# Performance work log

Hardware: AMD Instinct MI355X
Metric: run time of the kernel (lower is better)

## Reference

```python
import jax, jax.numpy as jnp
import numpy as np

DECAY = 0.99
EPSILON = 1e-05
BETA = 0.25  # vq_commitment_beta


def setup_inputs() -> dict:
    key = jax.random.key(0)
    k1, k2, k3, k4 = jax.random.split(key, 4)
    N, dim, K = 32768, 512, 8192
    init_range = 1.0 / np.sqrt(dim)
    emb_w = jax.random.uniform(k3, (K, 2 * dim), dtype=jnp.float32,
                               minval=-init_range, maxval=init_range)
    return {
        "z_real": jax.random.normal(k1, (N, dim), dtype=jnp.float32),
        "z_imag": jax.random.normal(k2, (N, dim), dtype=jnp.float32),
        "emb_w": emb_w,
        "ema_cluster_size": jnp.zeros((K,), dtype=jnp.float32),
        "ema_w": emb_w.copy(),
    }


def reference(z_real, z_imag, emb_w, ema_cluster_size, ema_w):
    N, dim = z_real.shape
    K = emb_w.shape[0]
    z_flat = jnp.concatenate([z_real, z_imag], axis=-1)  # [N, 2*dim]

    # squared euclidean distances [N, K]
    x_sq = jnp.sum(z_flat * z_flat, axis=1, keepdims=True)
    y_sq = jnp.sum(emb_w * emb_w, axis=1)
    d = jnp.maximum(x_sq + y_sq - 2.0 * (z_flat @ emb_w.T), 0.0)
    indices = jnp.argmin(d, axis=-1)  # [N]
    z_q = emb_w[indices]              # [N, 2*dim]

    # EMA codebook update (training-mode buffer math, no grads)
    n_total = jnp.zeros((K,), z_flat.dtype).at[indices].add(1.0)
    new_cluster_size = ema_cluster_size * DECAY + (1.0 - DECAY) * n_total
    cs = new_cluster_size + EPSILON
    cs = cs + (cs < 1.0).astype(cs.dtype)
    dw = jnp.zeros((K, 2 * dim), z_flat.dtype).at[indices].add(z_flat)  # encodings.T @ z_flat
    new_ema_w = ema_w * DECAY + (1.0 - DECAY) * dw
    new_w = jnp.clip(new_ema_w / cs[:, None], -5.0, 5.0)

    loss_sample = BETA * jnp.mean((z_q - z_flat) ** 2, axis=-1)  # [N]

    # straight-through (forward value == z_q)
    z_q_st = z_flat + jax.lax.stop_gradient(z_q - z_flat)

    probs = n_total / N
    norm_entropy = -jnp.sum(probs * jnp.log(probs + 1e-10)) / np.log(float(K))

    z_q_r = z_q_st[..., :dim]
    z_q_i = z_q_st[..., dim:]
    return (z_q_r, z_q_i, loss_sample, indices, norm_entropy,
            new_w, new_cluster_size, new_ema_w)
```

## Files before the change

kernel.cpp:

```cpp
#include <hip/hip_runtime.h>
#include <hip/hip_bf16.h>

#define NROWS 32768
#define DIM   512
#define D2    1024
#define KCODE 8192
#define DECAYF 0.99f
#define OMD    0.01f
#define CANDCAP 16
#define ZMAX 6.0f
#define IRANGE 0.04419417382415922f
#define MARGIN_P (9200 << 7)

typedef __attribute__((ext_vector_type(4))) int   v4i;
typedef __attribute__((ext_vector_type(16))) int  i32x16;

#define WS_EMB8T   0u
#define WS_YSQ     8388608u
#define WS_NINT    8421376u
#define WS_ENT     8454144u
#define WS_FIDX    10682384u
#define WS_OFF     10813456u
#define WS_CUR     10846224u
#define WS_ROWLIST 10878992u

#define OUT_ZQR  0
#define OUT_ZQI  16777216
#define OUT_LOSS 33554432
#define OUT_IDX  33587200
#define OUT_ENT  33619968
#define OUT_NEWW 33619969
#define OUT_NCS  42008577
#define OUT_NEMA 42016769
#define PAIRS_OFF (OUT_NEWW + 1)

__device__ __forceinline__ float wredf(float v) {
    #pragma unroll
    for (int o = 32; o > 0; o >>= 1) v += __shfl_down(v, o, 64);
    return v;
}

__device__ __forceinline__ double wredd(double v) {
    #pragma unroll
    for (int o = 32; o > 0; o >>= 1) v += __shfl_down(v, o, 64);
    return __shfl(v, 0, 64);
}

__device__ __forceinline__ double ulp32_of(double v) {
    return scalbn(1.0, ilogb(v) - 23);
}

__device__ __forceinline__ void gload_lds16(const void* g, void* l) {
    __builtin_amdgcn_global_load_lds(
        (const __attribute__((address_space(1))) unsigned int*)(g),
        (__attribute__((address_space(3))) unsigned int*)(l), 16, 0, 0);
}

__device__ __forceinline__ int q4(float4 v, float s) {
    int a = (int)rintf(fminf(fmaxf(v.x * s, -127.f), 127.f));
    int b = (int)rintf(fminf(fmaxf(v.y * s, -127.f), 127.f));
    int c = (int)rintf(fminf(fmaxf(v.z * s, -127.f), 127.f));
    int d = (int)rintf(fminf(fmaxf(v.w * s, -127.f), 127.f));
    return (a & 255) | ((b & 255) << 8) | ((c & 255) << 16) | ((d & 255) << 24);
}

__global__ __launch_bounds__(256) void prep_emb(const float* __restrict__ emb,
                                                char* __restrict__ emb8t,
                                                int* __restrict__ ysq) {
    int wave = threadIdx.x >> 6, lane = threadIdx.x & 63;
    int k = blockIdx.x * 4 + wave;
    const float4* src = (const float4*)(emb + (size_t)k * D2);
    const float es = 127.0f / IRANGE;
    const float sfac_inv = 1.0f / (2.0f * (ZMAX / 127.0f) * (IRANGE / 127.0f));
    float s = 0.f;
    float4 v0 = src[lane * 4 + 0];
    float4 v1 = src[lane * 4 + 1];
    float4 v2 = src[lane * 4 + 2];
    float4 v3 = src[lane * 4 + 3];
    s += v0.x*v0.x + v0.y*v0.y + v0.z*v0.z + v0.w*v0.w;
    s += v1.x*v1.x + v1.y*v1.y + v1.z*v1.z + v1.w*v1.w;
    s += v2.x*v2.x + v2.y*v2.y + v2.z*v2.z + v2.w*v2.w;
    s += v3.x*v3.x + v3.y*v3.y + v3.z*v3.z + v3.w*v3.w;
    v4i pk; pk[0] = q4(v0, es); pk[1] = q4(v1, es); pk[2] = q4(v2, es); pk[3] = q4(v3, es);
    v4i* dst = (v4i*)(emb8t + (size_t)(k >> 5) * 32768 + (size_t)lane * 512 + (k & 31) * 16);
    *dst = pk;
    s = wredf(s);
    if (lane == 0) ysq[k] = (int)rintf(s * sfac_inv);
}

__global__ __launch_bounds__(512, 2) void argmin_gemm(
    const float* __restrict__ zr, const float* __restrict__ zi,
    const char* __restrict__ emb8t, const int* __restrict__ ysq,
    long long* __restrict__ pairs)
{
    __shared__ char bufs[2][65536];
    const int tid  = threadIdx.x;
    const int wave = tid >> 6, lane = tid & 63;
    const int colc = lane & 31;
    const int hh   = lane >> 5;
    const int rowblk = blockIdx.x >> 1;
    const int slice  = blockIdx.x & 1;

    const int arow = rowblk * 256 + wave * 32 + colc;
    const float zs = 127.0f / ZMAX;
    const float* zrp = zr + (size_t)arow * 512 + hh * 16;
    const float* zip = zi + (size_t)arow * 512 + hh * 16;
    v4i afrag[32];
    #pragma unroll
    for (int ft = 0; ft < 16; ++ft) {
        const float4* p = (const float4*)(zrp + ft * 32);
        v4i a; a[0] = q4(p[0], zs); a[1] = q4(p[1], zs); a[2] = q4(p[2], zs); a[3] = q4(p[3], zs);
        afrag[ft] = a;
    }
    #pragma unroll
    for (int ft = 0; ft < 16; ++ft) {
        const float4* p = (const float4*)(zip + ft * 32);
        v4i a; a[0] = q4(p[0], zs); a[1] = q4(p[1], zs); a[2] = q4(p[2], zs); a[3] = q4(p[3], zs);
        afrag[16 + ft] = a;
    }

    int tv0[16], tv1[16];
    #pragma unroll
    for (int g = 0; g < 16; ++g) { tv0[g] = 0x7FFFFFFF; tv1[g] = 0x7FFFFFFF; }

    const char* gslice = emb8t + (size_t)slice * 128 * 32768;
    const int* yslice = ysq + slice * 4096;

#define STAGE(dstbuf, c_) do {                                                   \
        const char* gb = gslice + (size_t)(c_) * 65536 + wave * 8192             \
                       + (size_t)lane * 16;                                      \
        char* lb = (dstbuf) + wave * 8192;                                       \
        _Pragma("unroll")                                                        \
        for (int q = 0; q < 8; ++q)                                              \
            gload_lds16(gb + q * 1024, lb + q * 1024);                           \
    } while (0)

    const int boff = colc * 16 + hh * 512;

    STAGE(bufs[0], 0);
    __syncthreads();

    for (int c = 0; c < 64; ++c) {
        const int cur = c & 1;
        if (c + 1 < 64) STAGE(bufs[cur ^ 1], c + 1);
        int ysA = yslice[c * 64 + colc];
        int ysB = yslice[c * 64 + 32 + colc];

        const char* bb = &bufs[cur][0] + boff;
        i32x16 accA, accB;
        #pragma unroll
        for (int g = 0; g < 16; ++g) { accA[g] = 0; accB[g] = 0; }
        __builtin_amdgcn_s_setprio(1);
        #pragma unroll
        for (int m = 0; m < 32; ++m) {
            v4i bA = *(const v4i*)(bb + m * 1024);
            v4i bB = *(const v4i*)(bb + m * 1024 + 32768);
            accA = __builtin_amdgcn_mfma_i32_32x32x32_i8(afrag[m], bA, accA, 0, 0, 0);
            accB = __builtin_amdgcn_mfma_i32_32x32x32_i8(afrag[m], bB, accB, 0, 0, 0);
        }
        __builtin_amdgcn_s_setprio(0);

        const int idA = c * 2, idB = c * 2 + 1;
        #pragma unroll
        for (int g = 0; g < 16; ++g) {
            int pkA = ((ysA - accA[g]) << 7) | idA;
            tv1[g] = min(tv1[g], max(pkA, tv0[g]));
            tv0[g] = min(tv0[g], pkA);
            int pkB = ((ysB - accB[g]) << 7) | idB;
            tv1[g] = min(tv1[g], max(pkB, tv0[g]));
            tv0[g] = min(tv0[g], pkB);
        }
        __syncthreads();
    }
#undef STAGE

    #pragma unroll
    for (int g = 0; g < 16; ++g) {
        int rloc = (g & 3) + 8 * (g >> 2) + 4 * hh;
        int rowg = rowblk * 256 + wave * 32 + rloc;
        size_t base = (size_t)rowg * 128 + slice * 64 + colc * 2;
        int t0 = tv0[g], t1 = tv1[g];
        int code0 = slice * 4096 + (t0 & 127) * 32 + colc;
        int code1 = slice * 4096 + (t1 & 127) * 32 + colc;
        pairs[base + 0] = ((long long)(unsigned)code0 << 32) | (unsigned)t0;
        pairs[base + 1] = ((long long)(unsigned)code1 << 32) | (unsigned)t1;
    }
}

__global__ __launch_bounds__(256) void cleanup(
    const float* __restrict__ zr, const float* __restrict__ zi,
    const float* __restrict__ emb, const long long* __restrict__ pairs,
    int* __restrict__ fidx, int* __restrict__ nint, float* __restrict__ out)
{
    __shared__ int candlds[4][CANDCAP];
    int wave = threadIdx.x >> 6, lane = threadIdx.x & 63;
    int r = blockIdx.x * 4 + wave;

    const long long* pr = pairs + (size_t)r * 128;
    long long p0 = pr[lane];
    long long p1 = pr[64 + lane];
    int v0v = (int)(unsigned)p0;
    int i0  = (int)(p0 >> 32);
    int v1v = (int)(unsigned)p1;
    int i1  = (int)(p1 >> 32);
    int m = min(v0v, v1v);
    #pragma unroll
    for (int o = 32; o > 0; o >>= 1) m = min(m, __shfl_xor(m, o, 64));
    int lim = m + MARGIN_P;
    unsigned long long m0 = __ballot(v0v < lim);
    unsigned long long m1 = __ballot(v1v < lim);
    int t0 = __popcll(m0);
    int cnt = t0 + __popcll(m1);
    if (cnt > CANDCAP) cnt = CANDCAP;
    unsigned long long below = (lane == 63) ? 0xFFFFFFFFFFFFFFFFull >> 1
                                            : ((1ull << lane) - 1);
    if (v0v < lim) {
        int pos = __popcll(m0 & below);
        if (pos < CANDCAP) candlds[wave][pos] = i0;
    }
    if (v1v < lim) {
        int pos = t0 + __popcll(m1 & below);
        if (pos < CANDCAP) candlds[wave][pos] = i1;
    }
    int best = candlds[wave][0];

    float zreg[16];
    #pragma unroll
    for (int p = 0; p < 4; ++p) {
        int d4 = p * 64 + lane;
        const float4* zp = (d4 < 128) ? (const float4*)(zr + (size_t)r * 512)
                                      : ((const float4*)(zi + (size_t)r * 512) - 128);
        float4 zv = zp[d4];
        zreg[p * 4 + 0] = zv.x; zreg[p * 4 + 1] = zv.y;
        zreg[p * 4 + 2] = zv.z; zreg[p * 4 + 3] = zv.w;
    }

    if (cnt > 1) {
        double xs = 0.0;
        #pragma unroll
        for (int j = 0; j < 16; ++j) xs += (double)zreg[j] * (double)zreg[j];
        xs = wredd(xs);
        double uS = ulp32_of(xs);

        double bD = 1e300; int bi = 1 << 30;
        for (int i = 0; i < cnt; ++i) {
            int cdx = candlds[wave][i];
            const float4* ep = (const float4*)(emb + (size_t)cdx * 1024);
            double ys = 0.0, tt = 0.0;
            #pragma unroll
            for (int p = 0; p < 4; ++p) {
                float4 ev = ep[p * 64 + lane];
                float q0 = ev.x * ev.x, q1 = ev.y * ev.y, q2 = ev.z * ev.z, q3 = ev.w * ev.w;
                ys += (double)q0 + (double)q1 + (double)q2 + (double)q3;
                tt += (double)zreg[p * 4 + 0] * (double)ev.x
                    + (double)zreg[p * 4 + 1] * (double)ev.y
                    + (double)zreg[p * 4 + 2] * (double)ev.z
                    + (double)zreg[p * 4 + 3] * (double)ev.w;
            }
            ys = wredd(ys);
            tt = wredd(tt);
            float y32 = (float)ys;
            float t32 = (float)tt;
            double dex = xs + ys - 2.0 * tt;
            double ud = ulp32_of(dex);
            double D = rint((double)y32 / uS) * uS - rint(2.0 * (double)t32 / ud) * ud;
            if (D < bD || (D == bD && cdx < bi)) { bD = D; bi = cdx; }
        }
        best = bi;
    }

    const float4* ep = (const float4*)(emb + (size_t)best * 1024);
    float acc = 0.f;
    #pragma unroll
    for (int p = 0; p < 4; ++p) {
        int d4 = p * 64 + lane;
        float4 ev = ep[d4];
        float dx = ev.x - zreg[p * 4 + 0]; acc += dx * dx;
        float dy = ev.y - zreg[p * 4 + 1]; acc += dy * dy;
        float dz = ev.z - zreg[p * 4 + 2]; acc += dz * dz;
        float dw = ev.w - zreg[p * 4 + 3]; acc += dw * dw;
        float4* op = (d4 < 128) ? (float4*)(out + OUT_ZQR + (size_t)r * 512)
                                : ((float4*)(out + OUT_ZQI + (size_t)r * 512) - 128);
        op[d4] = ev;
    }
    acc = wredf(acc);
    if (lane == 0) {
        fidx[r] = best;
        out[OUT_IDX + r] = (float)best;
        out[OUT_LOSS + r] = 0.25f * acc * (1.f / 1024.f);
        atomicAdd(nint + best, 1);
    }
}

__global__ __launch_bounds__(256) void scan_codes(const int* __restrict__ nint,
                                                  int* __restrict__ off,
                                                  int* __restrict__ cur) {
    __shared__ int part[256];
    int tid = threadIdx.x;
    int base = tid * 32;
    int loc[32];
    int s = 0;
    #pragma unroll
    for (int j = 0; j < 32; ++j) { loc[j] = s; s += nint[base + j]; }
    part[tid] = s;
    __syncthreads();
    for (int o = 1; o < 256; o <<= 1) {
        int t = (tid >= o) ? part[tid - o] : 0;
        __syncthreads();
        part[tid] += t;
        __syncthreads();
    }
    int excl = part[tid] - s;
    #pragma unroll
    for (int j = 0; j < 32; ++j) {
        off[base + j] = excl + loc[j];
        cur[base + j] = 0;
    }
}

__global__ __launch_bounds__(256) void fill_rows(const int* __restrict__ fidx,
                                                 const int* __restrict__ off,
                                                 int* __restrict__ cur,
                                                 int* __restrict__ rowlist) {
    int r = blockIdx.x * 256 + threadIdx.x;
    int idx = fidx[r];
    int pos = atomicAdd(cur + idx, 1);
    rowlist[off[idx] + pos] = r;
}

__global__ __launch_bounds__(256) void ema_update(
    const float* __restrict__ zr, const float* __restrict__ zi,
    const float* __restrict__ emaw, const float* __restrict__ emacs,
    const int* __restrict__ nint, const int* __restrict__ off,
    const int* __restrict__ rowlist, float* __restrict__ out,
    float* __restrict__ entacc)
{
    int k = blockIdx.x;
    int tid = threadIdx.x;
    int cnt = nint[k];
    int o0 = off[k];
    float ax = 0.f, ay = 0.f, az = 0.f, aw = 0.f;
    for (int i = 0; i < cnt; ++i) {
        int r = rowlist[o0 + i];
        float4 zv = (tid < 128) ? ((const float4*)(zr + (size_t)r * 512))[tid]
                                : ((const float4*)(zi + (size_t)r * 512))[tid - 128];
        ax += zv.x; ay += zv.y; az += zv.z; aw += zv.w;
    }
    float4 ew = ((const float4*)(emaw + (size_t)k * 1024))[tid];
    float4 nem;
    nem.x = DECAYF * ew.x + OMD * ax;
    nem.y = DECAYF * ew.y + OMD * ay;
    nem.z = DECAYF * ew.z + OMD * az;
    nem.w = DECAYF * ew.w + OMD * aw;
    ((float4*)(out + OUT_NEMA + (size_t)k * 1024))[tid] = nem;
    float ncs = DECAYF * emacs[k] + OMD * (float)cnt;
    float cs = ncs + 1e-5f;
    if (cs < 1.f) cs += 1.f;
    float inv = 1.f / cs;
    float4 w;
    w.x = fminf(fmaxf(nem.x * inv, -5.f), 5.f);
    w.y = fminf(fmaxf(nem.y * inv, -5.f), 5.f);
    w.z = fminf(fmaxf(nem.z * inv, -5.f), 5.f);
    w.w = fminf(fmaxf(nem.w * inv, -5.f), 5.f);
    ((float4*)(out + OUT_NEWW + (size_t)k * 1024))[tid] = w;
    if (tid == 0) {
        out[OUT_NCS + k] = ncs;
        float p = (float)cnt / 32768.f;
        atomicAdd(entacc, -p * logf(p + 1e-10f));
    }
}

__global__ void ent_fin(const float* __restrict__ entacc, float* __restrict__ out) {
    if (threadIdx.x == 0) out[OUT_ENT] = entacc[0] / logf(8192.f);
}

extern "C" void kernel_launch(void* const* d_in, const int* in_sizes, int n_in,
                              void* d_out, int out_size, void* d_ws, size_t ws_size,
                              hipStream_t stream)
{
    const float* zr    = (const float*)d_in[0];
    const float* zi    = (const float*)d_in[1];
    const float* emb   = (const float*)d_in[2];
    const float* emacs = (const float*)d_in[3];
    const float* emaw  = (const float*)d_in[4];
    float* out = (float*)d_out;
    char* ws = (char*)d_ws;

    char*  emb8t   = (char*)(ws + WS_EMB8T);
    int*   ysq     = (int*)(ws + WS_YSQ);
    int*   nint    = (int*)(ws + WS_NINT);
    float* entacc  = (float*)(ws + WS_ENT);
    int*   fidx    = (int*)(ws + WS_FIDX);
    int*   off     = (int*)(ws + WS_OFF);
    int*   cur     = (int*)(ws + WS_CUR);
    int*   rowlist = (int*)(ws + WS_ROWLIST);
    long long* pairs = (long long*)(out + PAIRS_OFF);

    hipMemsetAsync(ws + WS_NINT, 0, 32768 + 16, stream);

    prep_emb   <<<2048, 256, 0, stream>>>(emb, emb8t, ysq);
    argmin_gemm<<<256,  512, 0, stream>>>(zr, zi, emb8t, ysq, pairs);
    cleanup    <<<8192, 256, 0, stream>>>(zr, zi, emb, pairs, fidx, nint, out);
    scan_codes <<<1,    256, 0, stream>>>(nint, off, cur);
    fill_rows  <<<128,  256, 0, stream>>>(fidx, off, cur, rowlist);
    ema_update <<<8192, 256, 0, stream>>>(zr, zi, emaw, emacs, nint, off, rowlist, out, entacc);
    ent_fin    <<<1,    64,  0, stream>>>(entacc, out);
}
```

Baseline: 518.1 us.

## Deepen argmin GEMM pipeline to four smaller LDS stages with split-K accumulators

The codebook staging in the int8 argmin GEMM moves from a double buffer of 64KB tiles to a 4-deep ring of 32KB tiles, each holding 32 codes. Each iteration now waits on vmcnt with a single barrier instead of a full __syncthreads pair, and keeps three loads in flight. The K dimension is split over two independent accumulators (even and odd k-steps) that are summed afterwards, so consecutive MFMAs do not depend on each other. The loop runs 128 iterations with half the work each, which adds barrier overhead per MFMA. The prefetch past the last tile wraps around and reloads tile 0, which is harmless but adds redundant loads.

```diff
diff --git a/kernel.cpp b/kernel.cpp
--- a/kernel.cpp
+++ b/kernel.cpp
@@ -93,7 +93,7 @@
     const char* __restrict__ emb8t, const int* __restrict__ ysq,
     long long* __restrict__ pairs)
 {
-    __shared__ char bufs[2][65536];
+    __shared__ char bufs[4][32768];
     const int tid  = threadIdx.x;
     const int wave = tid >> 6, lane = tid & 63;
     const int colc = lane & 31;
@@ -126,51 +126,49 @@
     const char* gslice = emb8t + (size_t)slice * 128 * 32768;
     const int* yslice = ysq + slice * 4096;
 
-#define STAGE(dstbuf, c_) do {                                                   \
-        const char* gb = gslice + (size_t)(c_) * 65536 + wave * 8192             \
+#define STAGE(bidx_, t_) do {                                                    \
+        const char* gb = gslice + (size_t)(t_) * 32768 + wave * 4096             \
                        + (size_t)lane * 16;                                      \
-        char* lb = (dstbuf) + wave * 8192;                                       \
-        _Pragma("unroll")                                                        \
-        for (int q = 0; q < 8; ++q)                                              \
-            gload_lds16(gb + q * 1024, lb + q * 1024);                           \
+        char* lb = &bufs[bidx_][0] + wave * 4096;                                \
+        gload_lds16(gb,        lb);                                              \
+        gload_lds16(gb + 1024, lb + 1024);                                       \
+        gload_lds16(gb + 2048, lb + 2048);                                       \
+        gload_lds16(gb + 3072, lb + 3072);                                       \
     } while (0)
 
     const int boff = colc * 16 + hh * 512;
 
-    STAGE(bufs[0], 0);
-    __syncthreads();
-
-    for (int c = 0; c < 64; ++c) {
-        const int cur = c & 1;
-        if (c + 1 < 64) STAGE(bufs[cur ^ 1], c + 1);
-        int ysA = yslice[c * 64 + colc];
-        int ysB = yslice[c * 64 + 32 + colc];
-
-        const char* bb = &bufs[cur][0] + boff;
-        i32x16 accA, accB;
+    STAGE(0, 0);
+    STAGE(1, 1);
+    STAGE(2, 2);
+
+    for (int h = 0; h < 128; ++h) {
+        asm volatile("s_waitcnt vmcnt(8) lgkmcnt(0)" ::: "memory");
+        __builtin_amdgcn_s_barrier();
+        __builtin_amdgcn_sched_barrier(0);
+        STAGE((h + 3) & 3, (h + 3) & 127);
+        int ysv = yslice[h * 32 + colc];
+
+        const char* bb = &bufs[h & 3][0] + boff;
+        i32x16 accP, accQ;
         #pragma unroll
-        for (int g = 0; g < 16; ++g) { accA[g] = 0; accB[g] = 0; }
+        for (int g = 0; g < 16; ++g) { accP[g] = 0; accQ[g] = 0; }
         __builtin_amdgcn_s_setprio(1);
         #pragma unroll
-        for (int m = 0; m < 32; ++m) {
-            v4i bA = *(const v4i*)(bb + m * 1024);
-            v4i bB = *(const v4i*)(bb + m * 1024 + 32768);
-            accA = __builtin_amdgcn_mfma_i32_32x32x32_i8(afrag[m], bA, accA, 0, 0, 0);
-            accB = __builtin_amdgcn_mfma_i32_32x32x32_i8(afrag[m], bB, accB, 0, 0, 0);
+        for (int m = 0; m < 16; ++m) {
+            v4i bP = *(const v4i*)(bb + (2 * m) * 1024);
+            v4i bQ = *(const v4i*)(bb + (2 * m + 1) * 1024);
+            accP = __builtin_amdgcn_mfma_i32_32x32x32_i8(afrag[2 * m],     bP, accP, 0, 0, 0);
+            accQ = __builtin_amdgcn_mfma_i32_32x32x32_i8(afrag[2 * m + 1], bQ, accQ, 0, 0, 0);
         }
         __builtin_amdgcn_s_setprio(0);
 
-        const int idA = c * 2, idB = c * 2 + 1;
         #pragma unroll
         for (int g = 0; g < 16; ++g) {
-            int pkA = ((ysA - accA[g]) << 7) | idA;
-            tv1[g] = min(tv1[g], max(pkA, tv0[g]));
-            tv0[g] = min(tv0[g], pkA);
-            int pkB = ((ysB - accB[g]) << 7) | idB;
-            tv1[g] = min(tv1[g], max(pkB, tv0[g]));
-            tv0[g] = min(tv0[g], pkB);
+            int pk = ((ysv - accP[g] - accQ[g]) << 7) | h;
+            tv1[g] = min(tv1[g], max(pk, tv0[g]));
+            tv0[g] = min(tv0[g], pk);
         }
-        __syncthreads();
     }
 #undef STAGE
 
```

Result: no change. 527.6 us (+1.8%).
